# Performance work log

Measured on AMD Instinct MI355X. Metric: run time of the kernel, lower is better.

Reference implementation:

```python
import jax, jax.numpy as jnp
import numpy as np
from functools import partial

DN = ('NCHW', 'OIHW', 'NCHW')

def conv2d(x, w, b, stride):
    y = jax.lax.conv_general_dilated(x, w, (stride, stride), 'VALID', dimension_numbers=DN)
    return y + b[None, :, None, None]

def squash(s, eps=1e-8):
    norm = jnp.linalg.norm(s, axis=-1, keepdims=True)
    return (norm ** 2 / (1 + norm ** 2)) * s / (norm + eps)

def setup_inputs() -> dict:
    key = jax.random.key(0)
    ks = jax.random.split(key, 10)
    B, H, W = 16, 32, 512
    F, CAPS, E, OD = 64, 8, 8, 16
    H1 = (H - 6) // 2 + 1          # 14
    W1 = (W - 6) // 2 + 1          # 254
    N = F * H1 * W1 // CAPS        # 28448
    s = 0.05
    return {
        'x': jax.random.normal(ks[0], (B, H, W), jnp.float32),
        'conv1_w': jax.random.normal(ks[1], (F, 1, 6, 6), jnp.float32) * s,
        'conv1_b': jnp.zeros((F,), jnp.float32),
        'conv2_w': jax.random.normal(ks[2], (F, F, 6, 6), jnp.float32) * s,
        'conv2_b': jnp.zeros((F,), jnp.float32),
        'conv3_w': jax.random.normal(ks[3], (F, 2 * F, 1, 1), jnp.float32) * s,
        'conv3_b': jnp.zeros((F,), jnp.float32),
        'pc_w': jax.random.normal(ks[4], (N, CAPS, CAPS), jnp.float32) * s,  # [N, in, out]
        'pc_b': jnp.zeros((N, CAPS), jnp.float32),
        'ec_w': jax.random.normal(ks[5], (N, E, OD, CAPS), jnp.float32),
    }

def reference(x, conv1_w, conv1_b, conv2_w, conv2_b, conv3_w, conv3_b, pc_w, pc_b, ec_w):
    CAPS = pc_w.shape[1]
    NUM_ITER = 3
    B = x.shape[0]
    h = x[:, None]                                  # [B,1,H,W]
    h = jax.nn.relu(conv2d(h, conv1_w, conv1_b, 2)) # [B,F,14,254]
    y = jnp.pad(h, ((0, 0), (0, 0), (2, 3), (2, 3)))  # ZeroPad2d((2,3,2,3))
    y = jax.nn.relu(conv2d(y, conv2_w, conv2_b, 1))
    h = jax.nn.relu(jnp.concatenate((h, y), axis=1))
    h = conv2d(h, conv3_w, conv3_b, 1)              # [B,F,14,254]
    u_in = h.reshape(B, -1, CAPS)                   # [B,N,caps_len]
    # PrimaryCaps: N independent Linear(caps,caps) -> one batched einsum
    u = jnp.einsum('bni,nio->bno', u_in, pc_w) + pc_b[None]
    # EmotionCaps: per-capsule prediction u_hat [B,N,E,out_dim]
    u_hat = jnp.einsum('neoi,bni->bneo', ec_w, u)
    N, E = ec_w.shape[0], ec_w.shape[1]
    b_log = jnp.zeros((B, N, E), u_hat.dtype)
    v = None
    for r in range(NUM_ITER):
        c = jax.nn.softmax(b_log, axis=2)           # [B,N,E]
        s = jnp.einsum('bne,bneo->beo', c, u_hat)   # [B,E,out_dim]
        v = squash(s)
        if r < NUM_ITER - 1:
            b_log = b_log + jnp.einsum('bneo,beo->bne', u_hat, v)
    return jnp.linalg.norm(v, axis=-1)              # [B,E]
```

## Files before the change

### kernel.cpp

```cpp
#include <hip/hip_runtime.h>
#include <hip/hip_bf16.h>
#include <math.h>

#define BB 16
#define H1 14
#define W1 254
#define HPH 19
#define HPW2 264
#define NCAP 28448
#define FLATSZ 227584

typedef __attribute__((ext_vector_type(8))) short bf16x8;
typedef __attribute__((ext_vector_type(4))) float f32x4;

__device__ __forceinline__ ushort f2bf(float f) {
  __hip_bfloat16 h = __float2bfloat16(f);
  return *(ushort*)&h;
}

__global__ __launch_bounds__(256) void prep_w(const float* __restrict__ w2, const float* __restrict__ w3,
                                              ushort* __restrict__ wb, float* __restrict__ w3t) {
  int idx = blockIdx.x * 256 + threadIdx.x;
  if (idx < 147456) {
    int co = idx / 2304; int rem = idx - co * 2304;
    int tap = rem >> 6; int ci = rem & 63;
    wb[idx] = f2bf(w2[(co * 64 + ci) * 36 + tap]);
  }
  if (idx < 8192) {
    int co = idx & 63; int c = idx >> 6;
    w3t[idx] = w3[co * 128 + c];
  }
}

__global__ __launch_bounds__(256) void conv1_k(const float* __restrict__ x, const float* __restrict__ w1,
                                               const float* __restrict__ b1, float* __restrict__ hc) {
  const int i = blockIdx.x, b = blockIdx.y;
  __shared__ float xs[6 * 512];
  __shared__ float wsh[2304];
  __shared__ float bsh[64];
  const int t = threadIdx.x;
  for (int idx = t; idx < 6 * 512; idx += 256) {
    int r = idx >> 9, c = idx & 511;
    xs[idx] = x[((size_t)b * 32 + 2 * i + r) * 512 + c];
  }
  for (int idx = t; idx < 2304; idx += 256) wsh[idx] = w1[idx];
  if (t < 64) bsh[t] = b1[t];
  __syncthreads();
  if (t < 254) {
    for (int c = 0; c < 64; c++) {
      float acc = bsh[c];
#pragma unroll
      for (int p = 0; p < 6; p++)
#pragma unroll
        for (int q = 0; q < 6; q++)
          acc = fmaf(xs[p * 512 + 2 * t + q], wsh[c * 36 + p * 6 + q], acc);
      acc = fmaxf(acc, 0.f);
      hc[(((size_t)b * 64 + c) * H1 + i) * W1 + t] = acc;
    }
  }
}

__global__ __launch_bounds__(256) void nhwc_k(const float* __restrict__ hc, ushort* __restrict__ hpc) {
  const int ct = blockIdx.x, i = blockIdx.y, b = blockIdx.z;
  const int c0 = ct * 64;
  __shared__ float ls[64 * 65];
  const int t = threadIdx.x;
  for (int idx = t; idx < 4096; idx += 256) {
    int ci = idx >> 6, cc = idx & 63;
    int c = c0 + cc;
    ls[ci * 65 + cc] = (c < W1) ? hc[(((size_t)b * 64 + ci) * H1 + i) * W1 + c] : 0.f;
  }
  __syncthreads();
  uint* outp = (uint*)hpc;
  for (int idx = t; idx < 2048; idx += 256) {
    int cc = idx >> 5, ci2 = idx & 31;
    int c = c0 + cc;
    if (c < W1) {
      float f0 = ls[(2 * ci2) * 65 + cc];
      float f1 = ls[(2 * ci2 + 1) * 65 + cc];
      uint pk = (uint)f2bf(f0) | ((uint)f2bf(f1) << 16);
      outp[(((size_t)b * HPH + 2 + i) * HPW2 + 2 + c) * 32 + ci2] = pk;
    }
  }
}

__device__ __forceinline__ void stage_b(const ushort* __restrict__ wb, ushort* __restrict__ bbuf,
                                        int tap, int w, int l) {
#pragma unroll
  for (int r = 0; r < 2; r++) {
    int v = r * 256 + w * 64 + l;
    int co = v >> 3, s = v & 7;
    int g = s ^ (co & 7);
    const ushort* gp = wb + co * 2304 + tap * 64 + g * 8;
    ushort* lp = bbuf + (size_t)(r * 256 + w * 64) * 8;
    __builtin_amdgcn_global_load_lds((const uint*)gp, (uint*)lp, 16, 0, 0);
  }
}

__global__ __launch_bounds__(256, 1) void conv2_mfma(const ushort* __restrict__ hpc,
                                                     const ushort* __restrict__ wb,
                                                     const float* __restrict__ b2, float* __restrict__ y) {
  const int b = blockIdx.z, i = blockIdx.y, j0 = blockIdx.x * 128;
  const int t = threadIdx.x;
  const int w = t >> 6, l = t & 63;
  const int lr = l & 15, quad = l >> 4;

  __shared__ ushort bls[2][4096];

  f32x4 acc[2][4];
#pragma unroll
  for (int mt = 0; mt < 2; mt++)
#pragma unroll
    for (int nt = 0; nt < 4; nt++) acc[mt][nt] = (f32x4){0.f, 0.f, 0.f, 0.f};

  const ushort* abase = hpc + (((size_t)b * HPH + i) * HPW2 + (j0 + w * 32 + lr)) * 64 + quad * 8;

  bf16x8 a0[2][2], a1[2][2];

#define ALOAD(dst, tap)                                                        \
  {                                                                            \
    const int p_ = (tap) / 6, q_ = (tap) % 6;                                  \
    const ushort* ap_ = abase + ((size_t)p_ * HPW2 + q_) * 64;                 \
    dst[0][0] = *(const bf16x8*)(ap_);                                         \
    dst[0][1] = *(const bf16x8*)(ap_ + 1024);                                  \
    dst[1][0] = *(const bf16x8*)(ap_ + 32);                                    \
    dst[1][1] = *(const bf16x8*)(ap_ + 32 + 1024);                             \
  }

#define COMPUTE(a, bp)                                                         \
  {                                                                            \
    _Pragma("unroll")                                                          \
    for (int ch = 0; ch < 2; ch++) {                                           \
      const int g2 = ch * 4 + quad;                                            \
      _Pragma("unroll")                                                        \
      for (int nt = 0; nt < 4; nt++) {                                         \
        const int co = nt * 16 + lr;                                           \
        bf16x8 bf = *(const bf16x8*)((bp) + co * 64 + ((g2 ^ (co & 7)) * 8));  \
        acc[0][nt] = __builtin_amdgcn_mfma_f32_16x16x32_bf16(a[ch][0], bf, acc[0][nt], 0, 0, 0); \
        acc[1][nt] = __builtin_amdgcn_mfma_f32_16x16x32_bf16(a[ch][1], bf, acc[1][nt], 0, 0, 0); \
      }                                                                        \
    }                                                                          \
  }

  stage_b(wb, &bls[0][0], 0, w, l);
  __syncthreads();
  ALOAD(a0, 0);

  for (int tp = 0; tp < 36; tp += 2) {
    stage_b(wb, &bls[1][0], tp + 1, w, l);
    ALOAD(a1, tp + 1);
    COMPUTE(a0, &bls[0][0]);
    __syncthreads();
    if (tp + 2 < 36) {
      stage_b(wb, &bls[0][0], tp + 2, w, l);
      ALOAD(a0, tp + 2);
    }
    COMPUTE(a1, &bls[1][0]);
    __syncthreads();
  }

#pragma unroll
  for (int nt = 0; nt < 4; nt++) {
    const int co = nt * 16 + lr;
    const float bias = b2[co];
    float* yrow = y + (((size_t)b * 64 + co) * H1 + i) * W1;
#pragma unroll
    for (int mt = 0; mt < 2; mt++) {
      const int jb = j0 + w * 32 + mt * 16 + quad * 4;
#pragma unroll
      for (int r = 0; r < 4; r++) {
        int j = jb + r;
        if (j < W1) yrow[j] = fmaxf(acc[mt][nt][r] + bias, 0.f);
      }
    }
  }
#undef ALOAD
#undef COMPUTE
}

__global__ __launch_bounds__(256) void conv3_k(const float* __restrict__ hc, const float* __restrict__ y,
                                               const float* __restrict__ w3t, const float* __restrict__ b3,
                                               float* __restrict__ out3) {
  const int b = blockIdx.z, i = blockIdx.y, j0 = blockIdx.x * 64;
  __shared__ float cs[32][64];
  __shared__ float wsh[32][64];
  const int t = threadIdx.x;
  const int cog = t >> 4, jg = t & 15;
  float acc[4][4];
#pragma unroll
  for (int a = 0; a < 4; a++)
#pragma unroll
    for (int j = 0; j < 4; j++) acc[a][j] = 0.f;

  for (int ch = 0; ch < 4; ch++) {
    __syncthreads();
    for (int idx = t; idx < 2048; idx += 256) {
      int cl = idx >> 6; int j = j0 + (idx & 63);
      int c = ch * 32 + cl;
      float v = 0.f;
      if (j < W1) {
        if (c < 64) v = hc[(((size_t)b * 64 + c) * H1 + i) * W1 + j];
        else        v = y[(((size_t)b * 64 + (c - 64)) * H1 + i) * W1 + j];
      }
      cs[cl][idx & 63] = v;
    }
    for (int idx = t; idx < 2048; idx += 256)
      wsh[idx >> 6][idx & 63] = w3t[(ch * 32 + (idx >> 6)) * 64 + (idx & 63)];
    __syncthreads();
#pragma unroll
    for (int c = 0; c < 32; c++) {
      float4 xv = *(const float4*)&cs[c][jg * 4];
      float4 wv = *(const float4*)&wsh[c][cog * 4];
#pragma unroll
      for (int jj = 0; jj < 4; jj++) {
        float xx = (&xv.x)[jj];
        acc[0][jj] = fmaf(wv.x, xx, acc[0][jj]);
        acc[1][jj] = fmaf(wv.y, xx, acc[1][jj]);
        acc[2][jj] = fmaf(wv.z, xx, acc[2][jj]);
        acc[3][jj] = fmaf(wv.w, xx, acc[3][jj]);
      }
    }
  }
#pragma unroll
  for (int a = 0; a < 4; a++) {
    int co = cog * 4 + a;
    float bias = b3[co];
#pragma unroll
    for (int jj = 0; jj < 4; jj++) {
      int j = j0 + jg * 4 + jj;
      if (j < W1) out3[(((size_t)b * 64 + co) * H1 + i) * W1 + j] = acc[a][jj] + bias;
    }
  }
}

__global__ __launch_bounds__(256) void pc_k(const float* __restrict__ out3, const float* __restrict__ pcw,
                                            const float* __restrict__ pcb, float* __restrict__ u) {
  int n = blockIdx.x * 256 + threadIdx.x;
  if (n >= NCAP) return;
  float pw[64];
  const float4* pwp = (const float4*)(pcw + (size_t)n * 64);
#pragma unroll
  for (int k = 0; k < 16; k++) {
    float4 v = pwp[k];
    pw[4 * k] = v.x; pw[4 * k + 1] = v.y; pw[4 * k + 2] = v.z; pw[4 * k + 3] = v.w;
  }
  float pb[8];
  {
    const float4* pbp = (const float4*)(pcb + (size_t)n * 8);
    float4 a = pbp[0], b = pbp[1];
    pb[0] = a.x; pb[1] = a.y; pb[2] = a.z; pb[3] = a.w;
    pb[4] = b.x; pb[5] = b.y; pb[6] = b.z; pb[7] = b.w;
  }
  for (int b = 0; b < BB; b++) {
    const float4* uip = (const float4*)(out3 + (size_t)b * FLATSZ + (size_t)n * 8);
    float4 a = uip[0], c = uip[1];
    float ui[8] = {a.x, a.y, a.z, a.w, c.x, c.y, c.z, c.w};
    float uo[8];
#pragma unroll
    for (int o = 0; o < 8; o++) uo[o] = pb[o];
#pragma unroll
    for (int i2 = 0; i2 < 8; i2++)
#pragma unroll
      for (int o = 0; o < 8; o++) uo[o] = fmaf(ui[i2], pw[i2 * 8 + o], uo[o]);
    float4* up = (float4*)(u + ((size_t)b * NCAP + n) * 8);
    up[0] = make_float4(uo[0], uo[1], uo[2], uo[3]);
    up[1] = make_float4(uo[4], uo[5], uo[6], uo[7]);
  }
}

__device__ __forceinline__ void block_reduce_atomic(float* __restrict__ sg, const float sacc[32], int t, int l, int wv) {
  __shared__ float red[8192];
#pragma unroll
  for (int k = 0; k < 32; k++) red[k * 256 + wv * 64 + l] = sacc[k];
  __syncthreads();
#pragma unroll
  for (int m = 0; m < 8; m++) {
    int slot = t + 256 * m;
    int b = slot >> 7, eo = slot & 127;
    int k = 2 * b + (eo & 1), l2 = eo >> 1;
    const float* r = red + k * 256 + l2;
    atomicAdd(&sg[slot], r[0] + r[64] + r[128] + r[192]);
  }
}

__global__ __launch_bounds__(256) void r0_k(const float* __restrict__ u, const float* __restrict__ ecw,
                                            float* __restrict__ s0) {
  const int t = threadIdx.x, l = t & 63, wv = t >> 6;
  const int nbase = blockIdx.x * 16 + wv * 4;
  float sacc[32];
#pragma unroll
  for (int k = 0; k < 32; k++) sacc[k] = 0.f;
  for (int c = 0; c < 4; c++) {
    const int n = nbase + c;
    float ec[16];
    const float4* ep = (const float4*)(ecw + (size_t)n * 1024 + l * 16);
#pragma unroll
    for (int k = 0; k < 4; k++) {
      float4 q = ep[k];
      ec[4 * k] = q.x; ec[4 * k + 1] = q.y; ec[4 * k + 2] = q.z; ec[4 * k + 3] = q.w;
    }
#pragma unroll
    for (int b = 0; b < BB; b++) {
      const float4* up = (const float4*)(u + ((size_t)b * NCAP + n) * 8);
      float4 ua = up[0], ubv = up[1];
      float uv[8] = {ua.x, ua.y, ua.z, ua.w, ubv.x, ubv.y, ubv.z, ubv.w};
      float h0 = 0.f, h1 = 0.f;
#pragma unroll
      for (int k = 0; k < 8; k++) { h0 = fmaf(ec[k], uv[k], h0); h1 = fmaf(ec[8 + k], uv[k], h1); }
      sacc[2 * b] += h0; sacc[2 * b + 1] += h1;
    }
  }
  block_reduce_atomic(s0, sacc, t, l, wv);
}

__global__ __launch_bounds__(256) void rr_k(const float* __restrict__ u, const float* __restrict__ ecw,
                                            const float* __restrict__ v, float* __restrict__ sout) {
  __shared__ float vlds[2048];
  const int t = threadIdx.x, l = t & 63, wv = t >> 6;
  for (int idx = t; idx < 2048; idx += 256) vlds[idx] = v[idx];
  __syncthreads();
  const int nbase = blockIdx.x * 16 + wv * 4;
  float sacc[32];
#pragma unroll
  for (int k = 0; k < 32; k++) sacc[k] = 0.f;
  for (int c = 0; c < 4; c++) {
    const int n = nbase + c;
    float ec[16];
    const float4* ep = (const float4*)(ecw + (size_t)n * 1024 + l * 16);
#pragma unroll
    for (int k = 0; k < 4; k++) {
      float4 q = ep[k];
      ec[4 * k] = q.x; ec[4 * k + 1] = q.y; ec[4 * k + 2] = q.z; ec[4 * k + 3] = q.w;
    }
#pragma unroll
    for (int bc = 0; bc < 2; bc++) {
      float uh0[8], uh1[8];
#pragma unroll
      for (int bb = 0; bb < 8; bb++) {
        const int b = bc * 8 + bb;
        const float4* up = (const float4*)(u + ((size_t)b * NCAP + n) * 8);
        float4 ua = up[0], ubv = up[1];
        float uv[8] = {ua.x, ua.y, ua.z, ua.w, ubv.x, ubv.y, ubv.z, ubv.w};
        float h0 = 0.f, h1 = 0.f;
#pragma unroll
        for (int k = 0; k < 8; k++) { h0 = fmaf(ec[k], uv[k], h0); h1 = fmaf(ec[8 + k], uv[k], h1); }
        uh0[bb] = h0; uh1[bb] = h1;
      }
#pragma unroll
      for (int bb = 0; bb < 8; bb++) {
        const int b = bc * 8 + bb;
        float2 vv = *(const float2*)&vlds[b * 128 + 2 * l];
        float p = uh0[bb] * vv.x + uh1[bb] * vv.y;
        p += __shfl_xor(p, 1); p += __shfl_xor(p, 2); p += __shfl_xor(p, 4);
        float m = p;
        m = fmaxf(m, __shfl_xor(m, 8)); m = fmaxf(m, __shfl_xor(m, 16)); m = fmaxf(m, __shfl_xor(m, 32));
        float ex = __expf(p - m);
        float den = ex;
        den += __shfl_xor(den, 8); den += __shfl_xor(den, 16); den += __shfl_xor(den, 32);
        float cc = ex * __builtin_amdgcn_rcpf(den);
        sacc[2 * b] = fmaf(cc, uh0[bb], sacc[2 * b]);
        sacc[2 * b + 1] = fmaf(cc, uh1[bb], sacc[2 * b + 1]);
      }
    }
  }
  block_reduce_atomic(sout, sacc, t, l, wv);
}

__global__ void squash_k(const float* __restrict__ s, float scale, const float* __restrict__ vprev,
                         float* __restrict__ vout) {
  int t = threadIdx.x;
  const float* sp = s + t * 16;
  float sv[16]; float nn = 0.f;
#pragma unroll
  for (int o = 0; o < 16; o++) { float x = sp[o] * scale; sv[o] = x; nn = fmaf(x, x, nn); }
  float norm = sqrtf(nn);
  float f = nn / (1.f + nn) / (norm + 1e-8f);
#pragma unroll
  for (int o = 0; o < 16; o++) {
    float base = vprev ? vprev[t * 16 + o] : 0.f;
    vout[t * 16 + o] = base + f * sv[o];
  }
}

__global__ void squash_out_k(const float* __restrict__ s, float* __restrict__ out) {
  int t = threadIdx.x;
  float nn = 0.f;
#pragma unroll
  for (int o = 0; o < 16; o++) { float x = s[t * 16 + o]; nn = fmaf(x, x, nn); }
  float norm = sqrtf(nn);
  float f = nn / (1.f + nn) / (norm + 1e-8f);
  out[t] = f * norm;
}

extern "C" void kernel_launch(void* const* d_in, const int* in_sizes, int n_in,
                              void* d_out, int out_size, void* d_ws, size_t ws_size,
                              hipStream_t stream) {
  const float* x   = (const float*)d_in[0];
  const float* w1  = (const float*)d_in[1];
  const float* b1  = (const float*)d_in[2];
  const float* w2  = (const float*)d_in[3];
  const float* b2  = (const float*)d_in[4];
  const float* w3  = (const float*)d_in[5];
  const float* b3  = (const float*)d_in[6];
  const float* pcw = (const float*)d_in[7];
  const float* pcb = (const float*)d_in[8];
  const float* ecw = (const float*)d_in[9];
  float* out = (float*)d_out;

  float* ws = (float*)d_ws;
  size_t o = 0;
  float* hc   = ws + o; o += 3641344;
  float* yb   = ws + o; o += 3641344;
  float* out3 = ws + o; o += 3641344;
  ushort* hpc = (ushort*)(ws + o); o += 2568192;
  ushort* wb  = (ushort*)(ws + o); o += 73728;
  float* w3t  = ws + o; o += 8192;
  float* s0   = ws + o; o += 2048;
  float* s1   = ws + o; o += 2048;
  float* s2   = ws + o; o += 2048;
  float* v0   = ws + o; o += 2048;
  float* v1   = ws + o; o += 2048;
  float* ub   = hc;

  hipMemsetAsync(hpc, 0, (size_t)16 * HPH * HPW2 * 64 * 2, stream);
  hipMemsetAsync(s0, 0, 3 * 2048 * 4, stream);

  prep_w<<<576, 256, 0, stream>>>(w2, w3, wb, w3t);
  conv1_k<<<dim3(14, 16), 256, 0, stream>>>(x, w1, b1, hc);
  nhwc_k<<<dim3(4, 14, 16), 256, 0, stream>>>(hc, hpc);
  conv2_mfma<<<dim3(2, 14, 16), 256, 0, stream>>>(hpc, wb, b2, yb);
  conv3_k<<<dim3(4, 14, 16), 256, 0, stream>>>(hc, yb, w3t, b3, out3);
  pc_k<<<112, 256, 0, stream>>>(out3, pcw, pcb, ub);
  r0_k<<<1778, 256, 0, stream>>>(ub, ecw, s0);
  squash_k<<<1, 128, 0, stream>>>(s0, 0.125f, nullptr, v0);
  rr_k<<<1778, 256, 0, stream>>>(ub, ecw, v0, s1);
  squash_k<<<1, 128, 0, stream>>>(s1, 1.0f, v0, v1);
  rr_k<<<1778, 256, 0, stream>>>(ub, ecw, v1, s2);
  squash_out_k<<<1, 128, 0, stream>>>(s2, out);
}
```

Before: 544.1 us.

## Merge routing kernels, split batch across grid, stage u in LDS

Replaces the separate r0/rr routing kernels with one templated route_k. Each block now covers 32 capsules and 8 batch entries, so the grid is split over two batch halves. Each wave stages its u slice in shared memory with coalesced loads instead of strided per-lane float4 global reads. The accumulator count halves to cut register pressure, with a launch_bounds occupancy hint. The trade-off is that the ec_w weights are now read twice, once per batch half, which doubles that global traffic.

```diff
diff --git a/kernel.cpp b/kernel.cpp
--- a/kernel.cpp
+++ b/kernel.cpp
@@ -268,89 +268,49 @@
   }
 }
 
-__device__ __forceinline__ void block_reduce_atomic(float* __restrict__ sg, const float sacc[32], int t, int l, int wv) {
-  __shared__ float red[8192];
-#pragma unroll
-  for (int k = 0; k < 32; k++) red[k * 256 + wv * 64 + l] = sacc[k];
-  __syncthreads();
-#pragma unroll
-  for (int m = 0; m < 8; m++) {
-    int slot = t + 256 * m;
-    int b = slot >> 7, eo = slot & 127;
-    int k = 2 * b + (eo & 1), l2 = eo >> 1;
-    const float* r = red + k * 256 + l2;
-    atomicAdd(&sg[slot], r[0] + r[64] + r[128] + r[192]);
-  }
-}
-
-__global__ __launch_bounds__(256) void r0_k(const float* __restrict__ u, const float* __restrict__ ecw,
-                                            float* __restrict__ s0) {
+template <int MODE>
+__global__ __launch_bounds__(256, 4) void route_k(const float* __restrict__ u, const float* __restrict__ ecw,
+                                                  const float* __restrict__ v, float* __restrict__ sout) {
   const int t = threadIdx.x, l = t & 63, wv = t >> 6;
-  const int nbase = blockIdx.x * 16 + wv * 4;
-  float sacc[32];
-#pragma unroll
-  for (int k = 0; k < 32; k++) sacc[k] = 0.f;
-  for (int c = 0; c < 4; c++) {
-    const int n = nbase + c;
-    float ec[16];
+  const int b0 = blockIdx.y * 8;
+  const int n0 = blockIdx.x * 32 + wv * 8;
+
+  __shared__ float us[4][512];
+  __shared__ float red[4096];
+  __shared__ float vlds[1024];
+
+  if (MODE) {
+    for (int idx = t; idx < 1024; idx += 256) vlds[idx] = v[b0 * 128 + idx];
+    __syncthreads();
+  }
+
+#pragma unroll
+  for (int bb = 0; bb < 8; bb++)
+    us[wv][bb * 64 + l] = u[((size_t)(b0 + bb) * NCAP + n0) * 8 + l];
+
+  float sacc[16];
+#pragma unroll
+  for (int k = 0; k < 16; k++) sacc[k] = 0.f;
+
+  for (int nn = 0; nn < 8; nn++) {
+    const int n = n0 + nn;
     const float4* ep = (const float4*)(ecw + (size_t)n * 1024 + l * 16);
-#pragma unroll
-    for (int k = 0; k < 4; k++) {
-      float4 q = ep[k];
-      ec[4 * k] = q.x; ec[4 * k + 1] = q.y; ec[4 * k + 2] = q.z; ec[4 * k + 3] = q.w;
-    }
-#pragma unroll
-    for (int b = 0; b < BB; b++) {
-      const float4* up = (const float4*)(u + ((size_t)b * NCAP + n) * 8);
+    float4 e0 = ep[0], e1 = ep[1], e2 = ep[2], e3 = ep[3];
+    float ec[16] = {e0.x, e0.y, e0.z, e0.w, e1.x, e1.y, e1.z, e1.w,
+                    e2.x, e2.y, e2.z, e2.w, e3.x, e3.y, e3.z, e3.w};
+#pragma unroll
+    for (int bb = 0; bb < 8; bb++) {
+      const float4* up = (const float4*)&us[wv][bb * 64 + nn * 8];
       float4 ua = up[0], ubv = up[1];
       float uv[8] = {ua.x, ua.y, ua.z, ua.w, ubv.x, ubv.y, ubv.z, ubv.w};
       float h0 = 0.f, h1 = 0.f;
 #pragma unroll
       for (int k = 0; k < 8; k++) { h0 = fmaf(ec[k], uv[k], h0); h1 = fmaf(ec[8 + k], uv[k], h1); }
-      sacc[2 * b] += h0; sacc[2 * b + 1] += h1;
-    }
-  }
-  block_reduce_atomic(s0, sacc, t, l, wv);
-}
-
-__global__ __launch_bounds__(256) void rr_k(const float* __restrict__ u, const float* __restrict__ ecw,
-                                            const float* __restrict__ v, float* __restrict__ sout) {
-  __shared__ float vlds[2048];
-  const int t = threadIdx.x, l = t & 63, wv = t >> 6;
-  for (int idx = t; idx < 2048; idx += 256) vlds[idx] = v[idx];
-  __syncthreads();
-  const int nbase = blockIdx.x * 16 + wv * 4;
-  float sacc[32];
-#pragma unroll
-  for (int k = 0; k < 32; k++) sacc[k] = 0.f;
-  for (int c = 0; c < 4; c++) {
-    const int n = nbase + c;
-    float ec[16];
-    const float4* ep = (const float4*)(ecw + (size_t)n * 1024 + l * 16);
-#pragma unroll
-    for (int k = 0; k < 4; k++) {
-      float4 q = ep[k];
-      ec[4 * k] = q.x; ec[4 * k + 1] = q.y; ec[4 * k + 2] = q.z; ec[4 * k + 3] = q.w;
-    }
-#pragma unroll
-    for (int bc = 0; bc < 2; bc++) {
-      float uh0[8], uh1[8];
-#pragma unroll
-      for (int bb = 0; bb < 8; bb++) {
-        const int b = bc * 8 + bb;
-        const float4* up = (const float4*)(u + ((size_t)b * NCAP + n) * 8);
-        float4 ua = up[0], ubv = up[1];
-        float uv[8] = {ua.x, ua.y, ua.z, ua.w, ubv.x, ubv.y, ubv.z, ubv.w};
-        float h0 = 0.f, h1 = 0.f;
-#pragma unroll
-        for (int k = 0; k < 8; k++) { h0 = fmaf(ec[k], uv[k], h0); h1 = fmaf(ec[8 + k], uv[k], h1); }
-        uh0[bb] = h0; uh1[bb] = h1;
-      }
-#pragma unroll
-      for (int bb = 0; bb < 8; bb++) {
-        const int b = bc * 8 + bb;
-        float2 vv = *(const float2*)&vlds[b * 128 + 2 * l];
-        float p = uh0[bb] * vv.x + uh1[bb] * vv.y;
+      if (MODE == 0) {
+        sacc[2 * bb] += h0; sacc[2 * bb + 1] += h1;
+      } else {
+        float2 vv = *(const float2*)&vlds[bb * 128 + 2 * l];
+        float p = h0 * vv.x + h1 * vv.y;
         p += __shfl_xor(p, 1); p += __shfl_xor(p, 2); p += __shfl_xor(p, 4);
         float m = p;
         m = fmaxf(m, __shfl_xor(m, 8)); m = fmaxf(m, __shfl_xor(m, 16)); m = fmaxf(m, __shfl_xor(m, 32));
@@ -358,12 +318,23 @@
         float den = ex;
         den += __shfl_xor(den, 8); den += __shfl_xor(den, 16); den += __shfl_xor(den, 32);
         float cc = ex * __builtin_amdgcn_rcpf(den);
-        sacc[2 * b] = fmaf(cc, uh0[bb], sacc[2 * b]);
-        sacc[2 * b + 1] = fmaf(cc, uh1[bb], sacc[2 * b + 1]);
+        sacc[2 * bb] = fmaf(cc, h0, sacc[2 * bb]);
+        sacc[2 * bb + 1] = fmaf(cc, h1, sacc[2 * bb + 1]);
       }
     }
   }
-  block_reduce_atomic(sout, sacc, t, l, wv);
+
+#pragma unroll
+  for (int k = 0; k < 16; k++) red[k * 256 + wv * 64 + l] = sacc[k];
+  __syncthreads();
+#pragma unroll
+  for (int m = 0; m < 4; m++) {
+    int slot = t + 256 * m;
+    int bl = slot >> 7, eo = slot & 127;
+    int k = 2 * bl + (eo & 1), l2 = eo >> 1;
+    const float* r = red + k * 256 + l2;
+    atomicAdd(&sout[(b0 + bl) * 128 + eo], r[0] + r[64] + r[128] + r[192]);
+  }
 }
 
 __global__ void squash_k(const float* __restrict__ s, float scale, const float* __restrict__ vprev,
@@ -431,10 +402,10 @@
   conv2_mfma<<<dim3(2, 14, 16), 256, 0, stream>>>(hpc, wb, b2, yb);
   conv3_k<<<dim3(4, 14, 16), 256, 0, stream>>>(hc, yb, w3t, b3, out3);
   pc_k<<<112, 256, 0, stream>>>(out3, pcw, pcb, ub);
-  r0_k<<<1778, 256, 0, stream>>>(ub, ecw, s0);
+  route_k<0><<<dim3(889, 2), 256, 0, stream>>>(ub, ecw, nullptr, s0);
   squash_k<<<1, 128, 0, stream>>>(s0, 0.125f, nullptr, v0);
-  rr_k<<<1778, 256, 0, stream>>>(ub, ecw, v0, s1);
+  route_k<1><<<dim3(889, 2), 256, 0, stream>>>(ub, ecw, v0, s1);
   squash_k<<<1, 128, 0, stream>>>(s1, 1.0f, v0, v1);
-  rr_k<<<1778, 256, 0, stream>>>(ub, ecw, v1, s2);
+  route_k<1><<<dim3(889, 2), 256, 0, stream>>>(ub, ecw, v1, s2);
   squash_out_k<<<1, 128, 0, stream>>>(s2, out);
 }
```

Result: faster. 495.6 us (-8.9%).
